# Optimization experiments

Hardware: AMD Instinct MI355X
Metric: run time of the kernel (lower is better)

Reference implementation:

```python
import jax, jax.numpy as jnp
import numpy as np


def setup_inputs() -> dict:
    key = jax.random.key(0)
    ks = jax.random.split(key, 4)
    b, n, d, dp = 8, 4096, 256, 512
    X = jax.random.normal(ks[0], (b, n, d), dtype=jnp.float32)
    P = jax.random.normal(ks[1], (b, n, d), dtype=jnp.float32)
    # linear hypernetwork params (Kaiming-ish scale)
    Wh1 = jax.random.normal(ks[2], (d, dp), dtype=jnp.float32) * (1.0 / np.sqrt(d))
    Wh2 = jax.random.normal(ks[3], (d, dp), dtype=jnp.float32) * (1.0 / np.sqrt(d))
    bh1 = jnp.zeros((dp,), dtype=jnp.float32)
    bh2 = jnp.zeros((dp,), dtype=jnp.float32)
    return {"X": X, "P": P, "Wh1": Wh1, "bh1": bh1, "Wh2": Wh2, "bh2": bh2}


def reference(X, P, Wh1, bh1, Wh2, bh2):
    # X, P: [b, n, d]
    Xp = X + P
    # hypernetwork-generated per-sample mixing weights: [b, n, d_prime]
    W1 = Xp @ Wh1 + bh1
    W2 = Xp @ Wh2 + bh2
    # token mixing: project tokens down to d_prime "mixing" space, GELU, back up
    Pm = jnp.einsum('bnp,bnd->bpd', W1, Xp)           # [b, d_prime, d]
    A = jax.nn.gelu(Pm, approximate=False)             # torch nn.GELU is exact erf form
    Y = jnp.einsum('bnp,bpd->bnd', W2, A)              # [b, n, d]
    return Y
```

## Files before the change

kernel.cpp:

```cpp
#include <hip/hip_runtime.h>

#define DEV static __device__ __forceinline__

typedef unsigned short u16;
typedef __bf16 bf16_t;
typedef __bf16 bf16x8 __attribute__((ext_vector_type(8)));
typedef float f32x4 __attribute__((ext_vector_type(4)));
typedef u16 u16x8 __attribute__((ext_vector_type(8)));

static constexpr int Bb = 8;
static constexpr int Nn = 4096;
static constexpr int Dd = 256;
static constexpr int DP = 512;

DEV void gload16(const void* g, void* l) {
  __builtin_amdgcn_global_load_lds(
      (__attribute__((address_space(1))) void*)(unsigned long long)(g),
      (__attribute__((address_space(3))) void*)(unsigned)(unsigned long long)(l),
      16, 0, 0);
}

DEV u16 f2bf(float x) { bf16_t h = (bf16_t)x; return __builtin_bit_cast(u16, h); }
DEV float bf2f(u16 v) { unsigned u = ((unsigned)v) << 16; return __builtin_bit_cast(float, u); }
DEV float gelu_exact(float x) { return 0.5f * x * (1.0f + erff(x * 0.70710678118654752f)); }

template <int NT>
DEV void gemm_tile(const u16* Ag, int lda, const u16* Bg, int ldb,
                   int k0, int ksteps, u16* ldsA, u16* ldsB, f32x4 acc[4][NT]) {
  const int tid  = threadIdx.x;
  const int wave = tid >> 6, lane = tid & 63;
  const int wr = wave >> 1, wc = wave & 1;
  const int lr = lane & 15, lk = (lane >> 4) * 8;
  const int srow = lane >> 2;
  const int skb  = (lane & 3) * 8;
  constexpr int BCH = NT / 2;
  constexpr int BBUF = NT * 1024;

  const int ca0 = wave * 2, ca1 = ca0 + 1;
  const size_t ga0 = (size_t)(ca0 * 16 + srow) * lda + skb;
  const size_t ga1 = (size_t)(ca1 * 16 + srow) * lda + skb;
  u16* la0 = ldsA + ca0 * 512; u16* la1 = ldsA + ca1 * 512;
  size_t gb[BCH]; u16* lb[BCH];
#pragma unroll
  for (int i = 0; i < BCH; ++i) {
    const int ch = wave * BCH + i;
    gb[i] = (size_t)(ch * 16 + srow) * ldb + skb;
    lb[i] = ldsB + ch * 512;
  }

  gload16(Ag + ga0 + k0, la0); gload16(Ag + ga1 + k0, la1);
#pragma unroll
  for (int i = 0; i < BCH; ++i) gload16(Bg + gb[i] + k0, lb[i]);
  asm volatile("s_waitcnt vmcnt(0)" ::: "memory");
  __syncthreads();

  int cur = 0;
  for (int kt = 0; kt < ksteps; ++kt) {
    const int nbuf = cur ^ 1;
    if (kt + 1 < ksteps) {
      const int kk = k0 + (kt + 1) * 32;
      gload16(Ag + ga0 + kk, la0 + nbuf * 4096);
      gload16(Ag + ga1 + kk, la1 + nbuf * 4096);
#pragma unroll
      for (int i = 0; i < BCH; ++i) gload16(Bg + gb[i] + kk, lb[i] + nbuf * BBUF);
    }
    const u16* pa = ldsA + cur * 4096;
    const u16* pb = ldsB + cur * BBUF;
    bf16x8 af[4], bfr[NT];
#pragma unroll
    for (int m = 0; m < 4; ++m)
      af[m] = *(const bf16x8*)(pa + (wr * 64 + m * 16 + lr) * 32 + lk);
#pragma unroll
    for (int n = 0; n < NT; ++n)
      bfr[n] = *(const bf16x8*)(pb + (wc * (NT * 16) + n * 16 + lr) * 32 + lk);
#pragma unroll
    for (int m = 0; m < 4; ++m)
#pragma unroll
      for (int n = 0; n < NT; ++n)
        acc[m][n] = __builtin_amdgcn_mfma_f32_16x16x32_bf16(af[m], bfr[n], acc[m][n], 0, 0, 0);
    asm volatile("s_waitcnt vmcnt(0)" ::: "memory");
    __syncthreads();
    cur = nbuf;
  }
}

template <int NT>
DEV void acc_zero(f32x4 acc[4][NT]) {
#pragma unroll
  for (int m = 0; m < 4; ++m)
#pragma unroll
    for (int n = 0; n < NT; ++n) {
      f32x4 z = {0.f, 0.f, 0.f, 0.f};
      acc[m][n] = z;
    }
}

__global__ __launch_bounds__(256) void k_s1(const float* __restrict__ X, const float* __restrict__ P,
                                            const float* __restrict__ Wh1, const float* __restrict__ Wh2,
                                            u16* __restrict__ Xp, u16* __restrict__ XpT,
                                            float* __restrict__ s_part,
                                            u16* __restrict__ WhT1, u16* __restrict__ Wbf2) {
  __shared__ u16 lt[64 * 65];
  const int bid = blockIdx.x;
  const int t = threadIdx.x;
  if (bid < 2048) {
    const int b  = bid >> 8;
    const int nt = (bid >> 2) & 63;
    const int dt = bid & 3;
    const int n0 = nt * 64, d0 = dt * 64;
    const int r = t >> 2, c0 = (t & 3) * 16;
    const size_t gbase = ((size_t)(b * Nn + n0 + r)) * Dd + d0 + c0;
    u16x8 lo, hi;
#pragma unroll
    for (int i = 0; i < 4; ++i) {
      float4 xv = *(const float4*)(X + gbase + i * 4);
      float4 pv = *(const float4*)(P + gbase + i * 4);
      u16 a0 = f2bf(xv.x + pv.x), a1 = f2bf(xv.y + pv.y);
      u16 a2 = f2bf(xv.z + pv.z), a3 = f2bf(xv.w + pv.w);
      if (i < 2) { lo[i*4+0]=a0; lo[i*4+1]=a1; lo[i*4+2]=a2; lo[i*4+3]=a3; }
      else       { int q=(i-2)*4; hi[q+0]=a0; hi[q+1]=a1; hi[q+2]=a2; hi[q+3]=a3; }
      lt[r * 65 + c0 + i*4 + 0] = a0; lt[r * 65 + c0 + i*4 + 1] = a1;
      lt[r * 65 + c0 + i*4 + 2] = a2; lt[r * 65 + c0 + i*4 + 3] = a3;
    }
    *(u16x8*)(Xp + gbase)     = lo;
    *(u16x8*)(Xp + gbase + 8) = hi;
    __syncthreads();
    const int dd = t >> 2, nc0 = (t & 3) * 16;
    u16x8 olo, ohi;
    float colsum = 0.f;
#pragma unroll
    for (int i = 0; i < 8; ++i) { olo[i] = lt[(nc0 + i) * 65 + dd]; colsum += bf2f(olo[i]); }
#pragma unroll
    for (int i = 0; i < 8; ++i) { ohi[i] = lt[(nc0 + 8 + i) * 65 + dd]; colsum += bf2f(ohi[i]); }
    const size_t obase = ((size_t)(b * Dd + d0 + dd)) * Nn + n0 + nc0;
    *(u16x8*)(XpT + obase)     = olo;
    *(u16x8*)(XpT + obase + 8) = ohi;
    colsum += __shfl_xor(colsum, 1);
    colsum += __shfl_xor(colsum, 2);
    if ((t & 3) == 0) s_part[(size_t)(b * 64 + nt) * Dd + d0 + dd] = colsum;
  } else if (bid < 2048 + 32) {
    const int wb = bid - 2048;
    const int rt = (wb >> 3) & 3;
    const int ct = wb & 7;
    const int r0 = rt * 64, c0t = ct * 64;
    const int r = t >> 2, c0 = (t & 3) * 16;
    const size_t gbase = (size_t)(r0 + r) * DP + c0t + c0;
#pragma unroll
    for (int i = 0; i < 4; ++i) {
      float4 v = *(const float4*)(Wh1 + gbase + i * 4);
      lt[r * 65 + c0 + i*4 + 0] = f2bf(v.x); lt[r * 65 + c0 + i*4 + 1] = f2bf(v.y);
      lt[r * 65 + c0 + i*4 + 2] = f2bf(v.z); lt[r * 65 + c0 + i*4 + 3] = f2bf(v.w);
    }
    __syncthreads();
    const int pp = t >> 2, dc0 = (t & 3) * 16;
    u16x8 olo, ohi;
#pragma unroll
    for (int i = 0; i < 8; ++i) olo[i] = lt[(dc0 + i) * 65 + pp];
#pragma unroll
    for (int i = 0; i < 8; ++i) ohi[i] = lt[(dc0 + 8 + i) * 65 + pp];
    u16* out = WhT1 + (size_t)(c0t + pp) * Dd + r0 + dc0;
    *(u16x8*)(out)     = olo;
    *(u16x8*)(out + 8) = ohi;
  } else {
    const int idx = ((bid - 2048 - 32) * 256 + t) * 8;
    float4 v0 = *(const float4*)(Wh2 + idx);
    float4 v1 = *(const float4*)(Wh2 + idx + 4);
    u16x8 o;
    o[0]=f2bf(v0.x); o[1]=f2bf(v0.y); o[2]=f2bf(v0.z); o[3]=f2bf(v0.w);
    o[4]=f2bf(v1.x); o[5]=f2bf(v1.y); o[6]=f2bf(v1.z); o[7]=f2bf(v1.w);
    *(u16x8*)(Wbf2 + idx) = o;
  }
}

__global__ __launch_bounds__(256) void k_gram(const u16* __restrict__ XpT, u16* __restrict__ G_part) {
  __shared__ __align__(16) u16 ldsA[2 * 128 * 32];
  __shared__ __align__(16) u16 ldsB[2 * 64 * 32];
  const int bid0 = blockIdx.x;
  const int bid = (bid0 & 7) * 64 + (bid0 >> 3);
  const int kc = bid & 7;
  const int tn = (bid >> 3) & 3;
  const int tm = (bid >> 5) & 1;
  const int b  = bid >> 6;
  const u16* Ag = XpT + (size_t)(b * Dd + tm * 128) * Nn;
  const u16* Bg = XpT + (size_t)(b * Dd + tn * 64) * Nn;
  f32x4 acc[4][2];
  acc_zero<2>(acc);
  gemm_tile<2>(Ag, Nn, Bg, Nn, kc * 512, 16, ldsA, ldsB, acc);
  const int tid = threadIdx.x, wave = tid >> 6, lane = tid & 63;
  const int wr = wave >> 1, wc = wave & 1, lr = lane & 15, lq = lane >> 4;
  u16* base = G_part + (size_t)kc * (Bb * Dd * Dd) + (size_t)(b * Dd + tm * 128) * Dd + tn * 64;
#pragma unroll
  for (int m = 0; m < 4; ++m)
#pragma unroll
    for (int n = 0; n < 2; ++n)
#pragma unroll
      for (int j = 0; j < 4; ++j)
        base[(size_t)(wr * 64 + m * 16 + lq * 4 + j) * Dd + wc * 32 + n * 16 + lr] =
            f2bf(acc[m][n][j]);
}

__global__ __launch_bounds__(256) void k_gsum(const u16* __restrict__ G_part,
                                              const float* __restrict__ s_part,
                                              u16* __restrict__ Gb, float* __restrict__ s,
                                              float* __restrict__ c) {
  const int bid = blockIdx.x;
  const int t = threadIdx.x;
  if (bid < 8) {
    const int b = bid, d = t;
    float sum = 0.f;
#pragma unroll 8
    for (int nt = 0; nt < 64; ++nt) sum += s_part[(size_t)(b * 64 + nt) * Dd + d];
    s[b * Dd + d] = sum;
    c[b * Dd + d] = 0.f;
  } else {
    const int e = ((bid - 8) * 256 + t) * 8;
    float a[8] = {0.f,0.f,0.f,0.f,0.f,0.f,0.f,0.f};
#pragma unroll
    for (int k = 0; k < 8; ++k) {
      u16x8 v = *(const u16x8*)(G_part + (size_t)k * (Bb * Dd * Dd) + e);
#pragma unroll
      for (int i = 0; i < 8; ++i) a[i] += bf2f(v[i]);
    }
    u16x8 o;
#pragma unroll
    for (int i = 0; i < 8; ++i) o[i] = f2bf(a[i]);
    *(u16x8*)(Gb + e) = o;
  }
}

__global__ __launch_bounds__(256) void k_pmAT(const u16* __restrict__ WhT1, const u16* __restrict__ Gb,
                                              const float* __restrict__ bh1, const float* __restrict__ s,
                                              const float* __restrict__ bh2,
                                              u16* __restrict__ AT, float* __restrict__ c) {
  __shared__ __align__(16) u16 ldsA[2 * 128 * 32];
  __shared__ __align__(16) u16 ldsB[2 * 128 * 32];
  __shared__ __align__(16) u16 ct[128 * 136];
  const int bid = blockIdx.x;
  const int tn = bid & 1;
  const int tm = (bid >> 1) & 3;
  const int b  = bid >> 3;
  const int p0 = tm * 128, d0 = tn * 128;
  const u16* Ag = WhT1 + (size_t)p0 * Dd;
  const u16* Bg = Gb + (size_t)(b * Dd + d0) * Dd;
  f32x4 acc[4][4];
  acc_zero<4>(acc);
  gemm_tile<4>(Ag, Dd, Bg, Dd, 0, Dd / 32, ldsA, ldsB, acc);
  const int tid = threadIdx.x, wave = tid >> 6, lane = tid & 63;
  const int wr = wave >> 1, wc = wave & 1, lr = lane & 15, lq = lane >> 4;
#pragma unroll
  for (int n = 0; n < 4; ++n) {
    const int col = wc * 64 + n * 16 + lr;
    const float sv = s[b * Dd + d0 + col];
#pragma unroll
    for (int m = 0; m < 4; ++m) {
#pragma unroll
      for (int j = 0; j < 4; ++j) {
        const int row = wr * 64 + m * 16 + lq * 4 + j;
        const float pm = acc[m][n][j] + bh1[p0 + row] * sv;
        ct[col * 136 + row] = f2bf(gelu_exact(pm));
      }
    }
  }
  __syncthreads();
#pragma unroll
  for (int it = 0; it < 8; ++it) {
    const int id = tid + it * 256;
    const int dl = id >> 4, ch = id & 15;
    *(u16x8*)(AT + (size_t)(b * Dd + d0 + dl) * DP + p0 + ch * 8) =
        *(const u16x8*)(ct + dl * 136 + ch * 8);
  }
  const int ccol = tid >> 1;
  const int chalf = tid & 1;
  float csum = 0.f;
#pragma unroll
  for (int q = 0; q < 8; ++q) {
    u16x8 av = *(const u16x8*)(ct + ccol * 136 + chalf * 64 + q * 8);
#pragma unroll
    for (int i = 0; i < 8; ++i) csum += bh2[p0 + chalf * 64 + q * 8 + i] * bf2f(av[i]);
  }
  csum += __shfl_xor(csum, 1);
  if (chalf == 0) atomicAdd(c + b * Dd + d0 + ccol, csum);
}

__global__ __launch_bounds__(256) void k_h(const u16* __restrict__ Wbf2, const u16* __restrict__ AT,
                                           u16* __restrict__ HT) {
  __shared__ __align__(16) u16 ldsA[2 * 128 * 32];
  __shared__ __align__(16) u16 ldsB[2 * 128 * 32];
  __shared__ __align__(16) u16 ct[128 * 136];
  const int bid = blockIdx.x;
  const int tn = bid & 1;
  const int tm = (bid >> 1) & 1;
  const int b  = bid >> 2;
  const int k0 = tm * 128, d0 = tn * 128;
  const u16* Ag = Wbf2 + (size_t)k0 * DP;
  const u16* Bg = AT + (size_t)(b * Dd + d0) * DP;
  f32x4 acc[4][4];
  acc_zero<4>(acc);
  gemm_tile<4>(Ag, DP, Bg, DP, 0, DP / 32, ldsA, ldsB, acc);
  const int tid = threadIdx.x, wave = tid >> 6, lane = tid & 63;
  const int wr = wave >> 1, wc = wave & 1, lr = lane & 15, lq = lane >> 4;
#pragma unroll
  for (int n = 0; n < 4; ++n) {
    const int col = wc * 64 + n * 16 + lr;
#pragma unroll
    for (int m = 0; m < 4; ++m)
#pragma unroll
      for (int j = 0; j < 4; ++j)
        ct[col * 136 + wr * 64 + m * 16 + lq * 4 + j] = f2bf(acc[m][n][j]);
  }
  __syncthreads();
#pragma unroll
  for (int it = 0; it < 8; ++it) {
    const int id = tid + it * 256;
    const int dl = id >> 4, ch = id & 15;
    *(u16x8*)(HT + (size_t)(b * Dd + d0 + dl) * Dd + k0 + ch * 8) =
        *(const u16x8*)(ct + dl * 136 + ch * 8);
  }
}

__global__ __launch_bounds__(256) void k_y(const u16* __restrict__ Xp, const u16* __restrict__ HT,
                                           const float* __restrict__ c, float* __restrict__ Y) {
  __shared__ __align__(16) u16 ldsA[2 * 128 * 32];
  __shared__ __align__(16) u16 ldsB[2 * 64 * 32];
  const int bid0 = blockIdx.x;
  const int bid = (bid0 & 7) * 128 + (bid0 >> 3);
  const int b  = bid >> 7;
  const int tm = (bid >> 2) & 31;
  const int tn = bid & 3;
  const u16* Ag = Xp + (size_t)(b * Nn + tm * 128) * Dd;
  const u16* Bg = HT + (size_t)(b * Dd + tn * 64) * Dd;
  f32x4 acc[4][2];
  acc_zero<2>(acc);
  gemm_tile<2>(Ag, Dd, Bg, Dd, 0, Dd / 32, ldsA, ldsB, acc);
  const int tid = threadIdx.x, wave = tid >> 6, lane = tid & 63;
  const int wr = wave >> 1, wc = wave & 1, lr = lane & 15, lq = lane >> 4;
  float* base = Y + (size_t)(b * Nn + tm * 128) * Dd + tn * 64;
#pragma unroll
  for (int n = 0; n < 2; ++n) {
    const int col = wc * 32 + n * 16 + lr;
    const float cv = c[b * Dd + tn * 64 + col];
#pragma unroll
    for (int m = 0; m < 4; ++m)
#pragma unroll
      for (int j = 0; j < 4; ++j)
        base[(size_t)(wr * 64 + m * 16 + lq * 4 + j) * Dd + col] = acc[m][n][j] + cv;
  }
}

extern "C" void kernel_launch(void* const* d_in, const int* in_sizes, int n_in,
                              void* d_out, int out_size, void* d_ws, size_t ws_size,
                              hipStream_t stream) {
  const float* X   = (const float*)d_in[0];
  const float* P   = (const float*)d_in[1];
  const float* Wh1 = (const float*)d_in[2];
  const float* bh1 = (const float*)d_in[3];
  const float* Wh2 = (const float*)d_in[4];
  const float* bh2 = (const float*)d_in[5];
  float* Y = (float*)d_out;
  char* ws = (char*)d_ws;

  u16*   Xp     = (u16*)(ws);
  u16*   XpT    = (u16*)(ws + 16777216);
  u16*   WhT1   = (u16*)(ws + 33554432);
  u16*   Wbf2   = (u16*)(ws + 33816576);
  u16*   G_part = (u16*)(ws + 34078720);
  float* s_part = (float*)(ws + 42467328);
  float* s      = (float*)(ws + 42991616);
  float* c      = (float*)(ws + 42999808);
  u16*   Gb     = (u16*)(ws + 43008000);
  u16*   AT     = (u16*)(ws + 44056576);
  u16*   HT     = (u16*)(ws + 46153728);
  const size_t WS_NEED = 47202304;
  if (ws_size < WS_NEED) return;

  k_s1  <<<2144, 256, 0, stream>>>(X, P, Wh1, Wh2, Xp, XpT, s_part, WhT1, Wbf2);
  k_gram<<<512,  256, 0, stream>>>(XpT, G_part);
  k_gsum<<<264,  256, 0, stream>>>(G_part, s_part, Gb, s, c);
  k_pmAT<<<64,   256, 0, stream>>>(WhT1, Gb, bh1, s, bh2, AT, c);
  k_h   <<<32,   256, 0, stream>>>(Wbf2, AT, HT);
  k_y   <<<1024, 256, 0, stream>>>(Xp, HT, c, Y);
}
```

Before: 72.14 us.

## Triple-buffer GEMM tile loads with partial vmcnt waits and alias epilogue LDS

Turns the double-buffered LDS pipeline in gemm_tile into a three-stage ring. Two k-steps are prefetched ahead, and each iteration waits only for the oldest stage using a partial vmcnt count instead of draining all loads. In k_pmAT and k_h, the epilogue staging buffer now aliases the operand buffers, so adding a third stage does not grow LDS there. This should hide more global-load latency, but it raises LDS use in k_gram and k_y and relies on hand-counted waitcnt values being correct.

```diff
diff --git a/kernel.cpp b/kernel.cpp
--- a/kernel.cpp
+++ b/kernel.cpp
@@ -27,15 +27,15 @@
 template <int NT>
 DEV void gemm_tile(const u16* Ag, int lda, const u16* Bg, int ldb,
                    int k0, int ksteps, u16* ldsA, u16* ldsB, f32x4 acc[4][NT]) {
+  constexpr int BCH  = NT / 2;
+  constexpr int ABUF = 4096;
+  constexpr int BBUF = NT * 1024;
   const int tid  = threadIdx.x;
   const int wave = tid >> 6, lane = tid & 63;
   const int wr = wave >> 1, wc = wave & 1;
   const int lr = lane & 15, lk = (lane >> 4) * 8;
   const int srow = lane >> 2;
   const int skb  = (lane & 3) * 8;
-  constexpr int BCH = NT / 2;
-  constexpr int BBUF = NT * 1024;
-
   const int ca0 = wave * 2, ca1 = ca0 + 1;
   const size_t ga0 = (size_t)(ca0 * 16 + srow) * lda + skb;
   const size_t ga1 = (size_t)(ca1 * 16 + srow) * lda + skb;
@@ -48,23 +48,27 @@
     lb[i] = ldsB + ch * 512;
   }
 
-  gload16(Ag + ga0 + k0, la0); gload16(Ag + ga1 + k0, la1);
-#pragma unroll
-  for (int i = 0; i < BCH; ++i) gload16(Bg + gb[i] + k0, lb[i]);
-  asm volatile("s_waitcnt vmcnt(0)" ::: "memory");
-  __syncthreads();
+  auto STAGE = [&](int kt, int buf) {
+    const int kk = k0 + kt * 32;
+    gload16(Ag + ga0 + kk, la0 + buf * ABUF);
+    gload16(Ag + ga1 + kk, la1 + buf * ABUF);
+#pragma unroll
+    for (int i = 0; i < BCH; ++i) gload16(Bg + gb[i] + kk, lb[i] + buf * BBUF);
+  };
+
+  STAGE(0, 0);
+  STAGE(1, 1);
+  if constexpr (NT == 2) asm volatile("s_waitcnt vmcnt(3)" ::: "memory");
+  else                   asm volatile("s_waitcnt vmcnt(4)" ::: "memory");
+  __builtin_amdgcn_s_barrier();
+  __builtin_amdgcn_sched_barrier(0);
 
   int cur = 0;
   for (int kt = 0; kt < ksteps; ++kt) {
-    const int nbuf = cur ^ 1;
-    if (kt + 1 < ksteps) {
-      const int kk = k0 + (kt + 1) * 32;
-      gload16(Ag + ga0 + kk, la0 + nbuf * 4096);
-      gload16(Ag + ga1 + kk, la1 + nbuf * 4096);
-#pragma unroll
-      for (int i = 0; i < BCH; ++i) gload16(Bg + gb[i] + kk, lb[i] + nbuf * BBUF);
-    }
-    const u16* pa = ldsA + cur * 4096;
+    const int sb = (cur + 2 >= 3) ? cur - 1 : cur + 2;
+    const bool do_stage = (kt + 2 < ksteps);
+    if (do_stage) STAGE(kt + 2, sb);
+    const u16* pa = ldsA + cur * ABUF;
     const u16* pb = ldsB + cur * BBUF;
     bf16x8 af[4], bfr[NT];
 #pragma unroll
@@ -78,10 +82,19 @@
 #pragma unroll
       for (int n = 0; n < NT; ++n)
         acc[m][n] = __builtin_amdgcn_mfma_f32_16x16x32_bf16(af[m], bfr[n], acc[m][n], 0, 0, 0);
-    asm volatile("s_waitcnt vmcnt(0)" ::: "memory");
-    __syncthreads();
-    cur = nbuf;
-  }
+    if (kt + 1 < ksteps) {
+      if (do_stage) {
+        if constexpr (NT == 2) asm volatile("s_waitcnt vmcnt(3)" ::: "memory");
+        else                   asm volatile("s_waitcnt vmcnt(4)" ::: "memory");
+      } else {
+        asm volatile("s_waitcnt vmcnt(0)" ::: "memory");
+      }
+      __builtin_amdgcn_s_barrier();
+      __builtin_amdgcn_sched_barrier(0);
+    }
+    cur = (cur + 1 == 3) ? 0 : cur + 1;
+  }
+  __builtin_amdgcn_s_barrier();
 }
 
 template <int NT>
@@ -173,8 +186,8 @@
 }
 
 __global__ __launch_bounds__(256) void k_gram(const u16* __restrict__ XpT, u16* __restrict__ G_part) {
-  __shared__ __align__(16) u16 ldsA[2 * 128 * 32];
-  __shared__ __align__(16) u16 ldsB[2 * 64 * 32];
+  __shared__ __align__(16) u16 ldsA[3 * 128 * 32];
+  __shared__ __align__(16) u16 ldsB[3 * 64 * 32];
   const int bid0 = blockIdx.x;
   const int bid = (bid0 & 7) * 64 + (bid0 >> 3);
   const int kc = bid & 7;
@@ -232,9 +245,10 @@
                                               const float* __restrict__ bh1, const float* __restrict__ s,
                                               const float* __restrict__ bh2,
                                               u16* __restrict__ AT, float* __restrict__ c) {
-  __shared__ __align__(16) u16 ldsA[2 * 128 * 32];
-  __shared__ __align__(16) u16 ldsB[2 * 128 * 32];
-  __shared__ __align__(16) u16 ct[128 * 136];
+  __shared__ __align__(16) u16 smem[24576];
+  u16* ldsA = smem;
+  u16* ldsB = smem + 12288;
+  u16* ct   = smem;
   const int bid = blockIdx.x;
   const int tn = bid & 1;
   const int tm = (bid >> 1) & 3;
@@ -284,9 +298,10 @@
 
 __global__ __launch_bounds__(256) void k_h(const u16* __restrict__ Wbf2, const u16* __restrict__ AT,
                                            u16* __restrict__ HT) {
-  __shared__ __align__(16) u16 ldsA[2 * 128 * 32];
-  __shared__ __align__(16) u16 ldsB[2 * 128 * 32];
-  __shared__ __align__(16) u16 ct[128 * 136];
+  __shared__ __align__(16) u16 smem[24576];
+  u16* ldsA = smem;
+  u16* ldsB = smem + 12288;
+  u16* ct   = smem;
   const int bid = blockIdx.x;
   const int tn = bid & 1;
   const int tm = (bid >> 1) & 1;
@@ -320,8 +335,8 @@
 
 __global__ __launch_bounds__(256) void k_y(const u16* __restrict__ Xp, const u16* __restrict__ HT,
                                            const float* __restrict__ c, float* __restrict__ Y) {
-  __shared__ __align__(16) u16 ldsA[2 * 128 * 32];
-  __shared__ __align__(16) u16 ldsB[2 * 64 * 32];
+  __shared__ __align__(16) u16 ldsA[3 * 128 * 32];
+  __shared__ __align__(16) u16 ldsB[3 * 64 * 32];
   const int bid0 = blockIdx.x;
   const int bid = (bid0 & 7) * 128 + (bid0 >> 3);
   const int b  = bid >> 7;
```

New measurement: 68.00 us. 1.06x faster.
